# Optimization experiments

Measured on AMD Instinct MI355X. Metric: run time of the kernel, lower is better.

## Reference

```python
import jax, jax.numpy as jnp
import numpy as np

ND, NPROT, E = 50000, 50000, 600000
DIN, DH, DO = 128, 128, 64


def setup_inputs() -> dict:
    key = jax.random.key(0)
    ks = jax.random.split(key, 16)
    s = 0.05
    inp = {
        "x_drug": jax.random.normal(ks[0], (ND, DIN), jnp.float32),
        "x_prot": jax.random.normal(ks[1], (NPROT, DIN), jnp.float32),
        "src_ddi": jax.random.randint(ks[2], (E,), 0, ND, dtype=jnp.int32),
        "dst_ddi": jax.random.randint(ks[3], (E,), 0, ND, dtype=jnp.int32),
        "src_dpi": jax.random.randint(ks[4], (E,), 0, ND, dtype=jnp.int32),
        "dst_dpi": jax.random.randint(ks[5], (E,), 0, NPROT, dtype=jnp.int32),
        "src_ppi": jax.random.randint(ks[6], (E,), 0, NPROT, dtype=jnp.int32),
        "dst_ppi": jax.random.randint(ks[7], (E,), 0, NPROT, dtype=jnp.int32),
        "W1_ddi": jax.random.normal(ks[8], (DIN, DH), jnp.float32) * s,
        "b1_ddi": jnp.zeros((DH,), jnp.float32),
        "W1_dpi": jax.random.normal(ks[9], (DIN, DH), jnp.float32) * s,
        "b1_dpi": jnp.zeros((DH,), jnp.float32),
        "W1_ppi": jax.random.normal(ks[10], (DIN, DH), jnp.float32) * s,
        "b1_ppi": jnp.zeros((DH,), jnp.float32),
        "W2_ddi": jax.random.normal(ks[11], (DH, DO), jnp.float32) * s,
        "b2_ddi": jnp.zeros((DO,), jnp.float32),
        "W2_dpi": jax.random.normal(ks[12], (DH, DO), jnp.float32) * s,
        "b2_dpi": jnp.zeros((DO,), jnp.float32),
        "W2_ppi": jax.random.normal(ks[13], (DH, DO), jnp.float32) * s,
        "b2_ppi": jnp.zeros((DO,), jnp.float32),
    }
    return inp


def _gconv(x_src, src, dst, W, b, n_dst):
    # GraphConv(norm='right'): transform, gather src, sum over in-edges, / in-degree, + bias
    h = x_src @ W                                    # [N_src, dout]
    agg = jax.ops.segment_sum(h[src], dst, num_segments=n_dst)  # [n_dst, dout]
    deg = jax.ops.segment_sum(jnp.ones(src.shape, h.dtype), dst, num_segments=n_dst)
    return agg / jnp.maximum(deg, 1.0)[:, None] + b


def reference(x_drug, x_prot, src_ddi, dst_ddi, src_dpi, dst_dpi, src_ppi, dst_ppi,
              W1_ddi, b1_ddi, W1_dpi, b1_dpi, W1_ppi, b1_ppi,
              W2_ddi, b2_ddi, W2_dpi, b2_dpi, W2_ppi, b2_ppi):
    nd, npr = x_drug.shape[0], x_prot.shape[0]
    # layer 1 (HeteroGraphConv: sum over relations per dst node type)
    h_d = _gconv(x_drug, src_ddi, dst_ddi, W1_ddi, b1_ddi, nd)
    h_p = (_gconv(x_drug, src_dpi, dst_dpi, W1_dpi, b1_dpi, npr)
           + _gconv(x_prot, src_ppi, dst_ppi, W1_ppi, b1_ppi, npr))
    # layer 2
    o_d = _gconv(h_d, src_ddi, dst_ddi, W2_ddi, b2_ddi, nd)
    o_p = (_gconv(h_d, src_dpi, dst_dpi, W2_dpi, b2_dpi, npr)
           + _gconv(h_p, src_ppi, dst_ppi, W2_ppi, b2_ppi, npr))
    # concat drug | protein outputs into one array
    return jnp.concatenate([o_d, o_p], axis=0)
```

## Files before the change

### kernel.cpp

```cpp
#include <hip/hip_runtime.h>

typedef unsigned int uint32;
typedef unsigned short ushort16;
typedef unsigned long long u64;
using short8 = __attribute__((ext_vector_type(8))) short;
using f32x4  = __attribute__((ext_vector_type(4))) float;

__device__ __forceinline__ float bfl(uint32 v) { return __uint_as_float(v << 16); }
__device__ __forceinline__ float bfh(uint32 v) { return __uint_as_float(v & 0xffff0000u); }
__device__ __forceinline__ ushort16 f2bf(float f) {
    uint32 u = __float_as_uint(f);
    u += 0x7fffu + ((u >> 16) & 1u);
    return (ushort16)(u >> 16);
}
__device__ __forceinline__ uint32 pack2(float x, float y) {
    return (uint32)f2bf(x) | ((uint32)f2bf(y) << 16);
}


constexpr int BIN_SH   = 10;
constexpr int CAP_PAIR = 16384;
constexpr int LCAP     = 48;
constexpr int NBIN_MAX = 160;

__global__ void init_ccur_kernel(int* __restrict__ ccur, int nbin) {
    int b = threadIdx.x;
    if (b < nbin) ccur[b] = b * CAP_PAIR;
}

__global__ __launch_bounds__(256) void part_a_kernel(
        const int* __restrict__ s0, const int* __restrict__ d0,
        const int* __restrict__ s1, const int* __restrict__ d1,
        const int* __restrict__ s2, const int* __restrict__ d2,
        int e0, int e01, int e012, int o1, int o2, int nbin,
        int* __restrict__ ccur, u64* __restrict__ cpair) {
    __shared__ u64 buf[NBIN_MAX][LCAP];
    __shared__ int lcnt[NBIN_MAX];
    const int tid = threadIdx.x;
    for (int b = tid; b < nbin; b += 256) lcnt[b] = 0;
    __syncthreads();
    const int step = gridDim.x * 1024;
    for (int base = blockIdx.x * 1024; base < e012; base += step) {
        #pragma unroll
        for (int k = 0; k < 4; ++k) {
            int i = base + tid + k * 256;
            if (i < e012) {
                int g, sv;
                if (i < e0)       { g = d0[i];            sv = s0[i]; }
                else if (i < e01) { g = o1 + d1[i - e0];  sv = s1[i - e0]; }
                else              { g = o2 + d2[i - e01]; sv = s2[i - e01]; }
                int bin = g >> BIN_SH;
                u64 pr = ((u64)(uint32)g << 32) | (uint32)sv;
                int slot = atomicAdd(&lcnt[bin], 1);
                if (slot < LCAP) {
                    buf[bin][slot] = pr;
                } else {
                    int p = atomicAdd(&ccur[bin], 1);
                    cpair[p] = pr;
                    atomicSub(&lcnt[bin], 1);
                }
            }
        }
        __syncthreads();
        if (tid < nbin) {
            int cnt = min(lcnt[tid], LCAP);
            if (cnt >= 32) {
                int n = cnt & ~31;
                int p = atomicAdd(&ccur[tid], n);
                for (int k = 0; k < n; ++k) cpair[p + k] = buf[tid][k];
                for (int k = 0; k < cnt - n; ++k) buf[tid][k] = buf[tid][n + k];
                lcnt[tid] = cnt - n;
            }
        }
        __syncthreads();
    }
    if (tid < nbin) {
        int cnt = min(lcnt[tid], LCAP);
        if (cnt > 0) {
            int p = atomicAdd(&ccur[tid], cnt);
            for (int k = 0; k < cnt; ++k) cpair[p + k] = buf[tid][k];
        }
    }
}

__global__ __launch_bounds__(64) void scan_bins_kernel(const int* __restrict__ ccur, int nbin,
                                                       int* __restrict__ cofs) {
    int lane = threadIdx.x;
    int run = 0;
    for (int base = 0; base < nbin; base += 64) {
        int b = base + lane;
        int c = (b < nbin) ? (ccur[b] - b * CAP_PAIR) : 0;
        int v = c;
        #pragma unroll
        for (int off = 1; off < 64; off <<= 1) {
            int u = __shfl_up(v, off);
            if (lane >= off) v += u;
        }
        if (b < nbin) cofs[b] = run + (v - c);
        run += __shfl(v, 63);
    }
    if (lane == 0) cofs[nbin] = run;
}

__global__ __launch_bounds__(256) void part_b_kernel(const u64* __restrict__ cpair,
                                                     const int* __restrict__ cofs,
                                                     int nbin, int tn, int e012,
                                                     int* __restrict__ rs,
                                                     int* __restrict__ esrc) {
    __shared__ int rs_l[1024];
    __shared__ int cur_l[1024];
    __shared__ int tsum[256];
    const int bin = blockIdx.x;
    const int t = threadIdx.x;
    const int g0 = bin << BIN_SH;
    const int gcnt = min(1024, tn - g0);
    const int pbase = bin * CAP_PAIR;
    const int obase = cofs[bin];
    const int cnt = cofs[bin + 1] - obase;
    #pragma unroll
    for (int k = 0; k < 4; ++k) cur_l[t + k * 256] = 0;
    __syncthreads();
    for (int i = t; i < cnt; i += 256) {
        int g = (int)(cpair[pbase + i] >> 32);
        atomicAdd(&cur_l[g - g0], 1);
    }
    __syncthreads();
    int v[4]; int s = 0;
    #pragma unroll
    for (int k = 0; k < 4; ++k) { v[k] = cur_l[t * 4 + k]; s += v[k]; }
    tsum[t] = s;
    __syncthreads();
    for (int off = 1; off < 256; off <<= 1) {
        int add = (t >= off) ? tsum[t - off] : 0;
        __syncthreads();
        tsum[t] += add;
        __syncthreads();
    }
    int run = (t ? tsum[t - 1] : 0);
    #pragma unroll
    for (int k = 0; k < 4; ++k) { rs_l[t * 4 + k] = run; run += v[k]; }
    __syncthreads();
    #pragma unroll
    for (int k = 0; k < 4; ++k) {
        int j = t + k * 256;
        if (j < gcnt) rs[g0 + j] = obase + rs_l[j];
    }
    if (bin == nbin - 1 && t == 0) rs[tn] = e012;
    #pragma unroll
    for (int k = 0; k < 4; ++k) cur_l[t + k * 256] = 0;
    __syncthreads();
    for (int i = t; i < cnt; i += 256) {
        u64 pr = cpair[pbase + i];
        int g = (int)(pr >> 32);
        int p = atomicAdd(&cur_l[g - g0], 1);
        esrc[obase + rs_l[g - g0] + p] = (int)(uint32)(pr & 0xffffffffu);
    }
}


struct CvtWArgs { const float* W[6]; ushort16* Wt[6]; };

__global__ void cvtW_all_kernel(CvtWArgs a) {
    int i = blockIdx.x * blockDim.x + threadIdx.x;
    if (i < 3 * 16384) {
        int m = i / 16384, idx = i % 16384;
        int n = idx >> 7, k = idx & 127;
        a.Wt[m][n * 128 + k] = f2bf(a.W[m][k * 128 + n]);
    } else {
        i -= 3 * 16384;
        if (i >= 3 * 8192) return;
        int m = 3 + i / 8192, idx = i % 8192;
        int n = idx >> 7, k = idx & 127;
        a.Wt[m][n * 128 + k] = f2bf(a.W[m][k * 64 + n]);
    }
}


struct Gemm3Args {
    const void* A[3];
    const ushort16* Wt[3];
    ushort16* Y[3];
    int N[3];
    int nb0, nb01;
};

template<int M, bool F32A>
__global__ __launch_bounds__(256) void gemm3_kernel(Gemm3Args g) {
    constexpr int NTW = M / 64;
    constexpr int CH  = M / 8;
    __shared__ short8 As[64 * 16];
    int b = blockIdx.x;
    int r = (b < g.nb0) ? 0 : ((b < g.nb01) ? 1 : 2);
    int bloc = b - ((r == 0) ? 0 : ((r == 1) ? g.nb0 : g.nb01));
    const int N = g.N[r];
    const int row0 = bloc * 64;
    const int tid = threadIdx.x;
    const int w = tid >> 6, l = tid & 63;
    const int lr = l & 15, lg = l >> 4;

    #pragma unroll
    for (int it = 0; it < 4; ++it) {
        int idx = it * 256 + tid;
        int row = idx >> 4, c = idx & 15;
        int grow = row0 + row;
        short8 v = {0, 0, 0, 0, 0, 0, 0, 0};
        if (grow < N) {
            if (F32A) {
                const float* gp = (const float*)g.A[r] + (size_t)grow * 128 + c * 8;
                float4 f0 = *(const float4*)gp;
                float4 f1 = *(const float4*)(gp + 4);
                v[0] = (short)f2bf(f0.x); v[1] = (short)f2bf(f0.y);
                v[2] = (short)f2bf(f0.z); v[3] = (short)f2bf(f0.w);
                v[4] = (short)f2bf(f1.x); v[5] = (short)f2bf(f1.y);
                v[6] = (short)f2bf(f1.z); v[7] = (short)f2bf(f1.w);
            } else {
                v = *(const short8*)((const ushort16*)g.A[r] + (size_t)grow * 128 + c * 8);
            }
        }
        As[row * 16 + (c ^ (row & 7))] = v;
    }
    __syncthreads();

    short8 bf[NTW][4];
    #pragma unroll
    for (int t = 0; t < NTW; ++t) {
        int n = w * (NTW * 16) + t * 16 + lr;
        const ushort16* wr = g.Wt[r] + (size_t)n * 128 + lg * 8;
        #pragma unroll
        for (int ks = 0; ks < 4; ++ks) bf[t][ks] = *(const short8*)(wr + ks * 32);
    }

    f32x4 acc[4][NTW];
    #pragma unroll
    for (int rt = 0; rt < 4; ++rt)
        #pragma unroll
        for (int t = 0; t < NTW; ++t) acc[rt][t] = (f32x4){0.f, 0.f, 0.f, 0.f};

    #pragma unroll
    for (int rt = 0; rt < 4; ++rt) {
        int row = rt * 16 + lr;
        short8 a[4];
        #pragma unroll
        for (int ks = 0; ks < 4; ++ks)
            a[ks] = As[row * 16 + ((lg + ks * 4) ^ (lr & 7))];
        #pragma unroll
        for (int t = 0; t < NTW; ++t)
            #pragma unroll
            for (int ks = 0; ks < 4; ++ks)
                acc[rt][t] = __builtin_amdgcn_mfma_f32_16x16x32_bf16(a[ks], bf[t][ks],
                                                                     acc[rt][t], 0, 0, 0);
    }

    __syncthreads();
    ushort16* Ys = (ushort16*)As;
    #pragma unroll
    for (int rt = 0; rt < 4; ++rt) {
        int row = rt * 16 + lg * 4;
        #pragma unroll
        for (int t = 0; t < NTW; ++t) {
            int col = w * (NTW * 16) + t * 16 + lr;
            int chx = (col >> 3);
            #pragma unroll
            for (int j = 0; j < 4; ++j) {
                int rr = row + j;
                Ys[rr * M + ((chx ^ (rr & 7)) << 3) + (col & 7)] = f2bf(acc[rt][t][j]);
            }
        }
    }
    __syncthreads();
    ushort16* Y = g.Y[r];
    #pragma unroll
    for (int it = 0; it < 64 * CH / 256; ++it) {
        int idx = it * 256 + tid;
        int row = idx / CH, c = idx % CH;
        int grow = row0 + row;
        if (grow < N) {
            short8 v = *(const short8*)&Ys[row * M + ((c ^ (row & 7)) << 3)];
            *(short8*)(Y + (size_t)grow * M + c * 8) = v;
        }
    }
}


__global__ __launch_bounds__(256) void agg1_kernel(const uint4* __restrict__ tbA,
                                                   const uint4* __restrict__ tbB,
                                                   const uint4* __restrict__ tbC,
                                                   const int* __restrict__ esrc,
                                                   const int* __restrict__ rs,
                                                   const float* __restrict__ bA,
                                                   const float* __restrict__ bB,
                                                   const float* __restrict__ bC,
                                                   uint4* __restrict__ hd,
                                                   uint4* __restrict__ hp,
                                                   int ND, int NP, int o1, int o2) {
    __shared__ int sidx[4][64];
    const int w = threadIdx.x >> 6;
    const int lane = threadIdx.x & 63;
    const int wid = blockIdx.x * 4 + w;
    const int q = lane >> 4, c = lane & 15;
    if (wid >= ND + NP) return;
    float acc[8];
    auto zero = [&]() {
        for (int k = 0; k < 8; ++k) acc[k] = 0.f;
    };
    auto gather = [&](const uint4* __restrict__ tb, int e0, int e1) {
        for (int base = e0; base < e1; base += 64) {
            int cnt = min(64, e1 - base);
            if (lane < cnt) sidx[w][lane] = esrc[base + lane];
            int j = q;
            for (; j + 4 < cnt; j += 8) {
                uint4 v0 = tb[(size_t)sidx[w][j] * 16 + c];
                uint4 v1 = tb[(size_t)sidx[w][j + 4] * 16 + c];
                acc[0] += bfl(v0.x) + bfl(v1.x);  acc[1] += bfh(v0.x) + bfh(v1.x);
                acc[2] += bfl(v0.y) + bfl(v1.y);  acc[3] += bfh(v0.y) + bfh(v1.y);
                acc[4] += bfl(v0.z) + bfl(v1.z);  acc[5] += bfh(v0.z) + bfh(v1.z);
                acc[6] += bfl(v0.w) + bfl(v1.w);  acc[7] += bfh(v0.w) + bfh(v1.w);
            }
            if (j < cnt) {
                uint4 v0 = tb[(size_t)sidx[w][j] * 16 + c];
                acc[0] += bfl(v0.x);  acc[1] += bfh(v0.x);
                acc[2] += bfl(v0.y);  acc[3] += bfh(v0.y);
                acc[4] += bfl(v0.z);  acc[5] += bfh(v0.z);
                acc[6] += bfl(v0.w);  acc[7] += bfh(v0.w);
            }
        }
        #pragma unroll
        for (int k = 0; k < 8; ++k) {
            acc[k] += __shfl_xor(acc[k], 16);
            acc[k] += __shfl_xor(acc[k], 32);
        }
    };
    if (wid < ND) {
        int e0 = rs[wid], e1 = rs[wid + 1];
        zero();
        gather(tbA, e0, e1);
        if (lane < 16) {
            float inv = 1.f / (float)max(e1 - e0, 1);
            float4 b0 = ((const float4*)bA)[c * 2];
            float4 b1 = ((const float4*)bA)[c * 2 + 1];
            hd[(size_t)wid * 16 + c] = make_uint4(
                pack2(acc[0] * inv + b0.x, acc[1] * inv + b0.y),
                pack2(acc[2] * inv + b0.z, acc[3] * inv + b0.w),
                pack2(acc[4] * inv + b1.x, acc[5] * inv + b1.y),
                pack2(acc[6] * inv + b1.z, acc[7] * inv + b1.w));
        }
    } else {
        int p = wid - ND;
        int g1 = o1 + p, g2 = o2 + p;
        int e0 = rs[g1], e1 = rs[g1 + 1];
        zero();
        gather(tbB, e0, e1);
        float res[8];
        float inv1 = 1.f / (float)max(e1 - e0, 1);
        #pragma unroll
        for (int k = 0; k < 8; ++k) res[k] = acc[k] * inv1;
        int f0 = rs[g2], f1 = rs[g2 + 1];
        zero();
        gather(tbC, f0, f1);
        if (lane < 16) {
            float inv2 = 1.f / (float)max(f1 - f0, 1);
            float4 bb0 = ((const float4*)bB)[c * 2];
            float4 bb1 = ((const float4*)bB)[c * 2 + 1];
            float4 bc0 = ((const float4*)bC)[c * 2];
            float4 bc1 = ((const float4*)bC)[c * 2 + 1];
            float r0 = res[0] + acc[0] * inv2 + bb0.x + bc0.x;
            float r1 = res[1] + acc[1] * inv2 + bb0.y + bc0.y;
            float r2 = res[2] + acc[2] * inv2 + bb0.z + bc0.z;
            float r3 = res[3] + acc[3] * inv2 + bb0.w + bc0.w;
            float r4 = res[4] + acc[4] * inv2 + bb1.x + bc1.x;
            float r5 = res[5] + acc[5] * inv2 + bb1.y + bc1.y;
            float r6 = res[6] + acc[6] * inv2 + bb1.z + bc1.z;
            float r7 = res[7] + acc[7] * inv2 + bb1.w + bc1.w;
            hp[(size_t)p * 16 + c] = make_uint4(pack2(r0, r1), pack2(r2, r3),
                                                pack2(r4, r5), pack2(r6, r7));
        }
    }
}

__global__ __launch_bounds__(256) void agg2_kernel(const uint4* __restrict__ tbA,
                                                   const uint4* __restrict__ tbB,
                                                   const uint4* __restrict__ tbC,
                                                   const int* __restrict__ esrc,
                                                   const int* __restrict__ rs,
                                                   const float* __restrict__ bA,
                                                   const float* __restrict__ bB,
                                                   const float* __restrict__ bC,
                                                   float* __restrict__ out,
                                                   int ND, int NP, int o1, int o2) {
    __shared__ int sidx[4][64];
    const int w = threadIdx.x >> 6;
    const int lane = threadIdx.x & 63;
    const int wid = blockIdx.x * 4 + w;
    const int e8 = lane >> 3, c = lane & 7;
    if (wid >= ND + NP) return;
    float acc[8];
    auto zero = [&]() {
        for (int k = 0; k < 8; ++k) acc[k] = 0.f;
    };
    auto gather = [&](const uint4* __restrict__ tb, int e0, int e1) {
        for (int base = e0; base < e1; base += 64) {
            int cnt = min(64, e1 - base);
            if (lane < cnt) sidx[w][lane] = esrc[base + lane];
            int j = e8;
            for (; j + 8 < cnt; j += 16) {
                uint4 v0 = tb[(size_t)sidx[w][j] * 8 + c];
                uint4 v1 = tb[(size_t)sidx[w][j + 8] * 8 + c];
                acc[0] += bfl(v0.x) + bfl(v1.x);  acc[1] += bfh(v0.x) + bfh(v1.x);
                acc[2] += bfl(v0.y) + bfl(v1.y);  acc[3] += bfh(v0.y) + bfh(v1.y);
                acc[4] += bfl(v0.z) + bfl(v1.z);  acc[5] += bfh(v0.z) + bfh(v1.z);
                acc[6] += bfl(v0.w) + bfl(v1.w);  acc[7] += bfh(v0.w) + bfh(v1.w);
            }
            if (j < cnt) {
                uint4 v0 = tb[(size_t)sidx[w][j] * 8 + c];
                acc[0] += bfl(v0.x);  acc[1] += bfh(v0.x);
                acc[2] += bfl(v0.y);  acc[3] += bfh(v0.y);
                acc[4] += bfl(v0.z);  acc[5] += bfh(v0.z);
                acc[6] += bfl(v0.w);  acc[7] += bfh(v0.w);
            }
        }
        #pragma unroll
        for (int k = 0; k < 8; ++k) {
            acc[k] += __shfl_xor(acc[k], 8);
            acc[k] += __shfl_xor(acc[k], 16);
            acc[k] += __shfl_xor(acc[k], 32);
        }
    };
    if (wid < ND) {
        int e0 = rs[wid], e1 = rs[wid + 1];
        zero();
        gather(tbA, e0, e1);
        if (lane < 8) {
            float inv = 1.f / (float)max(e1 - e0, 1);
            float4 b0 = ((const float4*)bA)[c * 2];
            float4 b1 = ((const float4*)bA)[c * 2 + 1];
            float4 r0, r1;
            r0.x = acc[0] * inv + b0.x; r0.y = acc[1] * inv + b0.y;
            r0.z = acc[2] * inv + b0.z; r0.w = acc[3] * inv + b0.w;
            r1.x = acc[4] * inv + b1.x; r1.y = acc[5] * inv + b1.y;
            r1.z = acc[6] * inv + b1.z; r1.w = acc[7] * inv + b1.w;
            float4* op = (float4*)out + (size_t)wid * 16 + c * 2;
            op[0] = r0; op[1] = r1;
        }
    } else {
        int p = wid - ND;
        int g1 = o1 + p, g2 = o2 + p;
        int e0 = rs[g1], e1 = rs[g1 + 1];
        zero();
        gather(tbB, e0, e1);
        float res[8];
        float inv1 = 1.f / (float)max(e1 - e0, 1);
        #pragma unroll
        for (int k = 0; k < 8; ++k) res[k] = acc[k] * inv1;
        int f0 = rs[g2], f1 = rs[g2 + 1];
        zero();
        gather(tbC, f0, f1);
        if (lane < 8) {
            float inv2 = 1.f / (float)max(f1 - f0, 1);
            float4 bb0 = ((const float4*)bB)[c * 2];
            float4 bb1 = ((const float4*)bB)[c * 2 + 1];
            float4 bc0 = ((const float4*)bC)[c * 2];
            float4 bc1 = ((const float4*)bC)[c * 2 + 1];
            float4 r0, r1;
            r0.x = res[0] + acc[0] * inv2 + bb0.x + bc0.x;
            r0.y = res[1] + acc[1] * inv2 + bb0.y + bc0.y;
            r0.z = res[2] + acc[2] * inv2 + bb0.z + bc0.z;
            r0.w = res[3] + acc[3] * inv2 + bb0.w + bc0.w;
            r1.x = res[4] + acc[4] * inv2 + bb1.x + bc1.x;
            r1.y = res[5] + acc[5] * inv2 + bb1.y + bc1.y;
            r1.z = res[6] + acc[6] * inv2 + bb1.z + bc1.z;
            r1.w = res[7] + acc[7] * inv2 + bb1.w + bc1.w;
            float4* op = (float4*)out + (size_t)(ND + p) * 16 + c * 2;
            op[0] = r0; op[1] = r1;
        }
    }
}


extern "C" void kernel_launch(void* const* d_in, const int* in_sizes, int n_in,
                              void* d_out, int out_size, void* d_ws, size_t ws_size,
                              hipStream_t stream) {
    const float* x_drug = (const float*)d_in[0];
    const float* x_prot = (const float*)d_in[1];
    const int* src[3] = { (const int*)d_in[2], (const int*)d_in[4], (const int*)d_in[6] };
    const int* dst[3] = { (const int*)d_in[3], (const int*)d_in[5], (const int*)d_in[7] };
    const float* W1[3] = { (const float*)d_in[8],  (const float*)d_in[10], (const float*)d_in[12] };
    const float* b1[3] = { (const float*)d_in[9],  (const float*)d_in[11], (const float*)d_in[13] };
    const float* W2[3] = { (const float*)d_in[14], (const float*)d_in[16], (const float*)d_in[18] };
    const float* b2[3] = { (const float*)d_in[15], (const float*)d_in[17], (const float*)d_in[19] };

    const int ND = in_sizes[0] / 128;
    const int NP = in_sizes[1] / 128;
    const int EC[3] = { in_sizes[2], in_sizes[4], in_sizes[6] };
    float* out = (float*)d_out;

    const int o1 = ND, o2 = ND + NP;
    const int TN = ND + 2 * NP;
    const int NBIN = (TN + (1 << BIN_SH) - 1) >> BIN_SH;
    const int e0c = EC[0], e01 = EC[0] + EC[1], e012 = EC[0] + EC[1] + EC[2];

    char* w = (char*)d_ws;
    ushort16* hd16 = (ushort16*)w; w += (size_t)ND * 128 * 2;
    ushort16* hp16 = (ushort16*)w; w += (size_t)NP * 128 * 2;
    ushort16* tbA  = (ushort16*)w; w += (size_t)ND * 128 * 2;
    ushort16* tbB  = (ushort16*)w; w += (size_t)ND * 128 * 2;
    ushort16* tbC  = (ushort16*)w; w += (size_t)NP * 128 * 2;
    ushort16* Wt[6];
    for (int r = 0; r < 3; ++r) { Wt[r] = (ushort16*)w; w += 128 * 128 * 2; }
    for (int r = 0; r < 3; ++r) { Wt[3 + r] = (ushort16*)w; w += 64 * 128 * 2; }
    int* ip = (int*)w;
    int* rs_all   = ip; ip += TN + 1;
    int* esrc_all = ip; ip += e012;
    int* ccur     = ip; ip += NBIN_MAX;
    int* cofs     = ip; ip += NBIN_MAX + 1;
    u64* cpair = (u64*)hd16;

    {
        CvtWArgs a;
        for (int r = 0; r < 3; ++r) { a.W[r] = W1[r]; a.W[3 + r] = W2[r]; }
        for (int r = 0; r < 6; ++r) a.Wt[r] = Wt[r];
        cvtW_all_kernel<<<(3 * 16384 + 3 * 8192 + 255) / 256, 256, 0, stream>>>(a);
    }

    init_ccur_kernel<<<1, 256, 0, stream>>>(ccur, NBIN);
    part_a_kernel<<<512, 256, 0, stream>>>(src[0], dst[0], src[1], dst[1], src[2], dst[2],
                                           e0c, e01, e012, o1, o2, NBIN, ccur, cpair);
    scan_bins_kernel<<<1, 64, 0, stream>>>(ccur, NBIN, cofs);
    part_b_kernel<<<NBIN, 256, 0, stream>>>(cpair, cofs, NBIN, TN, e012, rs_all, esrc_all);

    auto gb64 = [](int n) { return (n + 63) / 64; };
    auto ab = [](int n) { return (n + 3) / 4; };

    {
        Gemm3Args g;
        g.A[0] = x_drug; g.A[1] = x_drug; g.A[2] = x_prot;
        g.Wt[0] = Wt[0]; g.Wt[1] = Wt[1]; g.Wt[2] = Wt[2];
        g.Y[0] = tbA; g.Y[1] = tbB; g.Y[2] = tbC;
        g.N[0] = ND; g.N[1] = ND; g.N[2] = NP;
        g.nb0 = gb64(ND); g.nb01 = gb64(ND) * 2;
        int nblk = gb64(ND) * 2 + gb64(NP);
        gemm3_kernel<128, true><<<nblk, 256, 0, stream>>>(g);
    }
    agg1_kernel<<<ab(ND + NP), 256, 0, stream>>>((const uint4*)tbA, (const uint4*)tbB,
                                                 (const uint4*)tbC, esrc_all, rs_all,
                                                 b1[0], b1[1], b1[2],
                                                 (uint4*)hd16, (uint4*)hp16, ND, NP, o1, o2);

    {
        Gemm3Args g;
        g.A[0] = hd16; g.A[1] = hd16; g.A[2] = hp16;
        g.Wt[0] = Wt[3]; g.Wt[1] = Wt[4]; g.Wt[2] = Wt[5];
        g.Y[0] = tbA; g.Y[1] = tbB; g.Y[2] = tbC;
        g.N[0] = ND; g.N[1] = ND; g.N[2] = NP;
        g.nb0 = gb64(ND); g.nb01 = gb64(ND) * 2;
        int nblk = gb64(ND) * 2 + gb64(NP);
        gemm3_kernel<64, false><<<nblk, 256, 0, stream>>>(g);
    }
    agg2_kernel<<<ab(ND + NP), 256, 0, stream>>>((const uint4*)tbA, (const uint4*)tbB,
                                                 (const uint4*)tbC, esrc_all, rs_all,
                                                 b2[0], b2[1], b2[2],
                                                 out, ND, NP, o1, o2);
}
```

Baseline: 244.5 us.

## Replace buffered binning with histogram-scan-scatter and fuse scatter into layer-1 GEMM launch

Replaces the shared-memory buffered bin partition with a deterministic per-block histogram, a flat prefix scan, and an exact-offset scatter. The weight conversion is folded into the histogram kernel. The scatter blocks share one launch with the layer-1 GEMM blocks so the two independent workloads can overlap. This removes the init kernel and the fixed-capacity padded pair layout, at the cost of reading dst twice and running a single-block 1024-thread scan over about 40K counters.

```diff
diff --git a/kernel.cpp b/kernel.cpp
--- a/kernel.cpp
+++ b/kernel.cpp
@@ -19,160 +19,77 @@
 
 
 constexpr int BIN_SH   = 10;
-constexpr int CAP_PAIR = 16384;
-constexpr int LCAP     = 48;
 constexpr int NBIN_MAX = 160;
-
-__global__ void init_ccur_kernel(int* __restrict__ ccur, int nbin) {
-    int b = threadIdx.x;
-    if (b < nbin) ccur[b] = b * CAP_PAIR;
-}
-
-__global__ __launch_bounds__(256) void part_a_kernel(
-        const int* __restrict__ s0, const int* __restrict__ d0,
-        const int* __restrict__ s1, const int* __restrict__ d1,
-        const int* __restrict__ s2, const int* __restrict__ d2,
+constexpr int PG       = 256;
+
+struct CvtWArgs { const float* W[6]; ushort16* Wt[6]; };
+
+__global__ __launch_bounds__(256) void hist_cvtw_kernel(
+        const int* __restrict__ d0, const int* __restrict__ d1, const int* __restrict__ d2,
         int e0, int e01, int e012, int o1, int o2, int nbin,
-        int* __restrict__ ccur, u64* __restrict__ cpair) {
-    __shared__ u64 buf[NBIN_MAX][LCAP];
-    __shared__ int lcnt[NBIN_MAX];
+        int* __restrict__ cntmat, CvtWArgs a) {
+    __shared__ int hist[NBIN_MAX];
     const int tid = threadIdx.x;
-    for (int b = tid; b < nbin; b += 256) lcnt[b] = 0;
-    __syncthreads();
-    const int step = gridDim.x * 1024;
-    for (int base = blockIdx.x * 1024; base < e012; base += step) {
+    const int blk = blockIdx.x;
+    for (int b = tid; b < nbin; b += 256) hist[b] = 0;
+    __syncthreads();
+    const int step = PG * 1024;
+    for (int base = blk * 1024; base < e012; base += step) {
         #pragma unroll
         for (int k = 0; k < 4; ++k) {
             int i = base + tid + k * 256;
             if (i < e012) {
-                int g, sv;
-                if (i < e0)       { g = d0[i];            sv = s0[i]; }
-                else if (i < e01) { g = o1 + d1[i - e0];  sv = s1[i - e0]; }
-                else              { g = o2 + d2[i - e01]; sv = s2[i - e01]; }
-                int bin = g >> BIN_SH;
-                u64 pr = ((u64)(uint32)g << 32) | (uint32)sv;
-                int slot = atomicAdd(&lcnt[bin], 1);
-                if (slot < LCAP) {
-                    buf[bin][slot] = pr;
-                } else {
-                    int p = atomicAdd(&ccur[bin], 1);
-                    cpair[p] = pr;
-                    atomicSub(&lcnt[bin], 1);
-                }
-            }
-        }
-        __syncthreads();
-        if (tid < nbin) {
-            int cnt = min(lcnt[tid], LCAP);
-            if (cnt >= 32) {
-                int n = cnt & ~31;
-                int p = atomicAdd(&ccur[tid], n);
-                for (int k = 0; k < n; ++k) cpair[p + k] = buf[tid][k];
-                for (int k = 0; k < cnt - n; ++k) buf[tid][k] = buf[tid][n + k];
-                lcnt[tid] = cnt - n;
-            }
-        }
-        __syncthreads();
-    }
-    if (tid < nbin) {
-        int cnt = min(lcnt[tid], LCAP);
-        if (cnt > 0) {
-            int p = atomicAdd(&ccur[tid], cnt);
-            for (int k = 0; k < cnt; ++k) cpair[p + k] = buf[tid][k];
-        }
-    }
-}
-
-__global__ __launch_bounds__(64) void scan_bins_kernel(const int* __restrict__ ccur, int nbin,
-                                                       int* __restrict__ cofs) {
-    int lane = threadIdx.x;
-    int run = 0;
-    for (int base = 0; base < nbin; base += 64) {
-        int b = base + lane;
-        int c = (b < nbin) ? (ccur[b] - b * CAP_PAIR) : 0;
-        int v = c;
-        #pragma unroll
-        for (int off = 1; off < 64; off <<= 1) {
-            int u = __shfl_up(v, off);
-            if (lane >= off) v += u;
-        }
-        if (b < nbin) cofs[b] = run + (v - c);
-        run += __shfl(v, 63);
-    }
-    if (lane == 0) cofs[nbin] = run;
-}
-
-__global__ __launch_bounds__(256) void part_b_kernel(const u64* __restrict__ cpair,
-                                                     const int* __restrict__ cofs,
-                                                     int nbin, int tn, int e012,
-                                                     int* __restrict__ rs,
-                                                     int* __restrict__ esrc) {
-    __shared__ int rs_l[1024];
-    __shared__ int cur_l[1024];
-    __shared__ int tsum[256];
-    const int bin = blockIdx.x;
+                int g;
+                if (i < e0)       g = d0[i];
+                else if (i < e01) g = o1 + d1[i - e0];
+                else              g = o2 + d2[i - e01];
+                atomicAdd(&hist[g >> BIN_SH], 1);
+            }
+        }
+    }
+    __syncthreads();
+    for (int b = tid; b < nbin; b += 256) cntmat[b * PG + blk] = hist[b];
+    const int gid = blk * 256 + tid;
+    for (int i = gid; i < 3 * 16384 + 3 * 8192; i += PG * 256) {
+        if (i < 3 * 16384) {
+            int m = i / 16384, idx = i % 16384;
+            int n = idx >> 7, k = idx & 127;
+            a.Wt[m][n * 128 + k] = f2bf(a.W[m][k * 128 + n]);
+        } else {
+            int j = i - 3 * 16384;
+            int m = 3 + j / 8192, idx = j % 8192;
+            int n = idx >> 7, k = idx & 127;
+            a.Wt[m][n * 128 + k] = f2bf(a.W[m][k * 64 + n]);
+        }
+    }
+}
+
+__global__ __launch_bounds__(1024) void scanflat_kernel(const int* __restrict__ cntmat,
+                                                        int n, int nbin,
+                                                        int* __restrict__ soff,
+                                                        int* __restrict__ cofs) {
+    __shared__ int tsum[1024];
     const int t = threadIdx.x;
-    const int g0 = bin << BIN_SH;
-    const int gcnt = min(1024, tn - g0);
-    const int pbase = bin * CAP_PAIR;
-    const int obase = cofs[bin];
-    const int cnt = cofs[bin + 1] - obase;
-    #pragma unroll
-    for (int k = 0; k < 4; ++k) cur_l[t + k * 256] = 0;
-    __syncthreads();
-    for (int i = t; i < cnt; i += 256) {
-        int g = (int)(cpair[pbase + i] >> 32);
-        atomicAdd(&cur_l[g - g0], 1);
-    }
-    __syncthreads();
-    int v[4]; int s = 0;
-    #pragma unroll
-    for (int k = 0; k < 4; ++k) { v[k] = cur_l[t * 4 + k]; s += v[k]; }
+    const int vpt = (n + 1023) >> 10;
+    const int lo = min(t * vpt, n);
+    const int hi = min(lo + vpt, n);
+    int s = 0;
+    for (int i = lo; i < hi; ++i) s += cntmat[i];
     tsum[t] = s;
     __syncthreads();
-    for (int off = 1; off < 256; off <<= 1) {
+    for (int off = 1; off < 1024; off <<= 1) {
         int add = (t >= off) ? tsum[t - off] : 0;
         __syncthreads();
         tsum[t] += add;
         __syncthreads();
     }
     int run = (t ? tsum[t - 1] : 0);
-    #pragma unroll
-    for (int k = 0; k < 4; ++k) { rs_l[t * 4 + k] = run; run += v[k]; }
-    __syncthreads();
-    #pragma unroll
-    for (int k = 0; k < 4; ++k) {
-        int j = t + k * 256;
-        if (j < gcnt) rs[g0 + j] = obase + rs_l[j];
-    }
-    if (bin == nbin - 1 && t == 0) rs[tn] = e012;
-    #pragma unroll
-    for (int k = 0; k < 4; ++k) cur_l[t + k * 256] = 0;
-    __syncthreads();
-    for (int i = t; i < cnt; i += 256) {
-        u64 pr = cpair[pbase + i];
-        int g = (int)(pr >> 32);
-        int p = atomicAdd(&cur_l[g - g0], 1);
-        esrc[obase + rs_l[g - g0] + p] = (int)(uint32)(pr & 0xffffffffu);
-    }
-}
-
-
-struct CvtWArgs { const float* W[6]; ushort16* Wt[6]; };
-
-__global__ void cvtW_all_kernel(CvtWArgs a) {
-    int i = blockIdx.x * blockDim.x + threadIdx.x;
-    if (i < 3 * 16384) {
-        int m = i / 16384, idx = i % 16384;
-        int n = idx >> 7, k = idx & 127;
-        a.Wt[m][n * 128 + k] = f2bf(a.W[m][k * 128 + n]);
-    } else {
-        i -= 3 * 16384;
-        if (i >= 3 * 8192) return;
-        int m = 3 + i / 8192, idx = i % 8192;
-        int n = idx >> 7, k = idx & 127;
-        a.Wt[m][n * 128 + k] = f2bf(a.W[m][k * 64 + n]);
-    }
+    for (int i = lo; i < hi; ++i) {
+        soff[i] = run;
+        if ((i & (PG - 1)) == 0) cofs[i / PG] = run;
+        run += cntmat[i];
+    }
+    if (t == 1023) cofs[nbin] = tsum[1023];
 }
 
 
@@ -185,11 +102,10 @@
 };
 
 template<int M, bool F32A>
-__global__ __launch_bounds__(256) void gemm3_kernel(Gemm3Args g) {
+__device__ __forceinline__ void gemm3_body(const Gemm3Args& g, int b, char* smem) {
     constexpr int NTW = M / 64;
     constexpr int CH  = M / 8;
-    __shared__ short8 As[64 * 16];
-    int b = blockIdx.x;
+    short8* As = (short8*)smem;
     int r = (b < g.nb0) ? 0 : ((b < g.nb01) ? 1 : 2);
     int bloc = b - ((r == 0) ? 0 : ((r == 1) ? g.nb0 : g.nb01));
     const int N = g.N[r];
@@ -252,7 +168,7 @@
     }
 
     __syncthreads();
-    ushort16* Ys = (ushort16*)As;
+    ushort16* Ys = (ushort16*)smem;
     #pragma unroll
     for (int rt = 0; rt < 4; ++rt) {
         int row = rt * 16 + lg * 4;
@@ -278,6 +194,101 @@
             short8 v = *(const short8*)&Ys[row * M + ((c ^ (row & 7)) << 3)];
             *(short8*)(Y + (size_t)grow * M + c * 8) = v;
         }
+    }
+}
+
+template<int M, bool F32A>
+__global__ __launch_bounds__(256) void a3gemm_kernel(
+        const int* __restrict__ s0, const int* __restrict__ d0,
+        const int* __restrict__ s1, const int* __restrict__ d1,
+        const int* __restrict__ s2, const int* __restrict__ d2,
+        int e0, int e01, int e012, int o1, int o2, int nbin,
+        const int* __restrict__ soff, u64* __restrict__ cpair,
+        Gemm3Args g) {
+    __shared__ char smem[16384];
+    const int tid = threadIdx.x;
+    if (blockIdx.x < PG) {
+        int* lcnt = (int*)smem;
+        const int blk = blockIdx.x;
+        for (int b = tid; b < nbin; b += 256) lcnt[b] = soff[b * PG + blk];
+        __syncthreads();
+        const int step = PG * 1024;
+        for (int base = blk * 1024; base < e012; base += step) {
+            #pragma unroll
+            for (int k = 0; k < 4; ++k) {
+                int i = base + tid + k * 256;
+                if (i < e012) {
+                    int gg, sv;
+                    if (i < e0)       { gg = d0[i];            sv = s0[i]; }
+                    else if (i < e01) { gg = o1 + d1[i - e0];  sv = s1[i - e0]; }
+                    else              { gg = o2 + d2[i - e01]; sv = s2[i - e01]; }
+                    int p = atomicAdd(&lcnt[gg >> BIN_SH], 1);
+                    cpair[p] = ((u64)(uint32)gg << 32) | (uint32)sv;
+                }
+            }
+        }
+    } else {
+        gemm3_body<M, F32A>(g, blockIdx.x - PG, smem);
+    }
+}
+
+template<int M, bool F32A>
+__global__ __launch_bounds__(256) void gemm3_kernel(Gemm3Args g) {
+    __shared__ char smem[16384];
+    gemm3_body<M, F32A>(g, blockIdx.x, smem);
+}
+
+__global__ __launch_bounds__(256) void part_b_kernel(const u64* __restrict__ cpair,
+                                                     const int* __restrict__ cofs,
+                                                     int nbin, int tn, int e012,
+                                                     int* __restrict__ rs,
+                                                     int* __restrict__ esrc) {
+    __shared__ int rs_l[1024];
+    __shared__ int cur_l[1024];
+    __shared__ int tsum[256];
+    const int bin = blockIdx.x;
+    const int t = threadIdx.x;
+    const int g0 = bin << BIN_SH;
+    const int gcnt = min(1024, tn - g0);
+    const int pbase = cofs[bin];
+    const int cnt = cofs[bin + 1] - pbase;
+    #pragma unroll
+    for (int k = 0; k < 4; ++k) cur_l[t + k * 256] = 0;
+    __syncthreads();
+    for (int i = t; i < cnt; i += 256) {
+        int g = (int)(cpair[pbase + i] >> 32);
+        atomicAdd(&cur_l[g - g0], 1);
+    }
+    __syncthreads();
+    int v[4]; int s = 0;
+    #pragma unroll
+    for (int k = 0; k < 4; ++k) { v[k] = cur_l[t * 4 + k]; s += v[k]; }
+    tsum[t] = s;
+    __syncthreads();
+    for (int off = 1; off < 256; off <<= 1) {
+        int add = (t >= off) ? tsum[t - off] : 0;
+        __syncthreads();
+        tsum[t] += add;
+        __syncthreads();
+    }
+    int run = (t ? tsum[t - 1] : 0);
+    #pragma unroll
+    for (int k = 0; k < 4; ++k) { rs_l[t * 4 + k] = run; run += v[k]; }
+    __syncthreads();
+    #pragma unroll
+    for (int k = 0; k < 4; ++k) {
+        int j = t + k * 256;
+        if (j < gcnt) rs[g0 + j] = pbase + rs_l[j];
+    }
+    if (bin == nbin - 1 && t == 0) rs[tn] = e012;
+    #pragma unroll
+    for (int k = 0; k < 4; ++k) cur_l[t + k * 256] = 0;
+    __syncthreads();
+    for (int i = t; i < cnt; i += 256) {
+        u64 pr = cpair[pbase + i];
+        int g = (int)(pr >> 32);
+        int p = atomicAdd(&cur_l[g - g0], 1);
+        esrc[pbase + rs_l[g - g0] + p] = (int)(uint32)(pr & 0xffffffffu);
     }
 }
 
@@ -510,51 +521,49 @@
     int* ip = (int*)w;
     int* rs_all   = ip; ip += TN + 1;
     int* esrc_all = ip; ip += e012;
-    int* ccur     = ip; ip += NBIN_MAX;
+    int* cntmat   = ip; ip += NBIN_MAX * PG;
+    int* soff     = ip; ip += NBIN_MAX * PG;
     int* cofs     = ip; ip += NBIN_MAX + 1;
     u64* cpair = (u64*)hd16;
 
-    {
-        CvtWArgs a;
-        for (int r = 0; r < 3; ++r) { a.W[r] = W1[r]; a.W[3 + r] = W2[r]; }
-        for (int r = 0; r < 6; ++r) a.Wt[r] = Wt[r];
-        cvtW_all_kernel<<<(3 * 16384 + 3 * 8192 + 255) / 256, 256, 0, stream>>>(a);
-    }
-
-    init_ccur_kernel<<<1, 256, 0, stream>>>(ccur, NBIN);
-    part_a_kernel<<<512, 256, 0, stream>>>(src[0], dst[0], src[1], dst[1], src[2], dst[2],
-                                           e0c, e01, e012, o1, o2, NBIN, ccur, cpair);
-    scan_bins_kernel<<<1, 64, 0, stream>>>(ccur, NBIN, cofs);
-    part_b_kernel<<<NBIN, 256, 0, stream>>>(cpair, cofs, NBIN, TN, e012, rs_all, esrc_all);
-
     auto gb64 = [](int n) { return (n + 63) / 64; };
     auto ab = [](int n) { return (n + 3) / 4; };
 
-    {
-        Gemm3Args g;
-        g.A[0] = x_drug; g.A[1] = x_drug; g.A[2] = x_prot;
-        g.Wt[0] = Wt[0]; g.Wt[1] = Wt[1]; g.Wt[2] = Wt[2];
-        g.Y[0] = tbA; g.Y[1] = tbB; g.Y[2] = tbC;
-        g.N[0] = ND; g.N[1] = ND; g.N[2] = NP;
-        g.nb0 = gb64(ND); g.nb01 = gb64(ND) * 2;
-        int nblk = gb64(ND) * 2 + gb64(NP);
-        gemm3_kernel<128, true><<<nblk, 256, 0, stream>>>(g);
-    }
+    CvtWArgs cw;
+    for (int r = 0; r < 3; ++r) { cw.W[r] = W1[r]; cw.W[3 + r] = W2[r]; }
+    for (int r = 0; r < 6; ++r) cw.Wt[r] = Wt[r];
+    hist_cvtw_kernel<<<PG, 256, 0, stream>>>(dst[0], dst[1], dst[2],
+                                             e0c, e01, e012, o1, o2, NBIN, cntmat, cw);
+
+    scanflat_kernel<<<1, 1024, 0, stream>>>(cntmat, NBIN * PG, NBIN, soff, cofs);
+
+    Gemm3Args g1;
+    g1.A[0] = x_drug; g1.A[1] = x_drug; g1.A[2] = x_prot;
+    g1.Wt[0] = Wt[0]; g1.Wt[1] = Wt[1]; g1.Wt[2] = Wt[2];
+    g1.Y[0] = tbA; g1.Y[1] = tbB; g1.Y[2] = tbC;
+    g1.N[0] = ND; g1.N[1] = ND; g1.N[2] = NP;
+    g1.nb0 = gb64(ND); g1.nb01 = gb64(ND) * 2;
+    int nblk1 = gb64(ND) * 2 + gb64(NP);
+    a3gemm_kernel<128, true><<<PG + nblk1, 256, 0, stream>>>(
+        src[0], dst[0], src[1], dst[1], src[2], dst[2],
+        e0c, e01, e012, o1, o2, NBIN, soff, cpair, g1);
+
+    part_b_kernel<<<NBIN, 256, 0, stream>>>(cpair, cofs, NBIN, TN, e012, rs_all, esrc_all);
+
     agg1_kernel<<<ab(ND + NP), 256, 0, stream>>>((const uint4*)tbA, (const uint4*)tbB,
                                                  (const uint4*)tbC, esrc_all, rs_all,
                                                  b1[0], b1[1], b1[2],
                                                  (uint4*)hd16, (uint4*)hp16, ND, NP, o1, o2);
 
-    {
-        Gemm3Args g;
-        g.A[0] = hd16; g.A[1] = hd16; g.A[2] = hp16;
-        g.Wt[0] = Wt[3]; g.Wt[1] = Wt[4]; g.Wt[2] = Wt[5];
-        g.Y[0] = tbA; g.Y[1] = tbB; g.Y[2] = tbC;
-        g.N[0] = ND; g.N[1] = ND; g.N[2] = NP;
-        g.nb0 = gb64(ND); g.nb01 = gb64(ND) * 2;
-        int nblk = gb64(ND) * 2 + gb64(NP);
-        gemm3_kernel<64, false><<<nblk, 256, 0, stream>>>(g);
-    }
+    Gemm3Args g2;
+    g2.A[0] = hd16; g2.A[1] = hd16; g2.A[2] = hp16;
+    g2.Wt[0] = Wt[3]; g2.Wt[1] = Wt[4]; g2.Wt[2] = Wt[5];
+    g2.Y[0] = tbA; g2.Y[1] = tbB; g2.Y[2] = tbC;
+    g2.N[0] = ND; g2.N[1] = ND; g2.N[2] = NP;
+    g2.nb0 = gb64(ND); g2.nb01 = gb64(ND) * 2;
+    int nblk2 = gb64(ND) * 2 + gb64(NP);
+    gemm3_kernel<64, false><<<nblk2, 256, 0, stream>>>(g2);
+
     agg2_kernel<<<ab(ND + NP), 256, 0, stream>>>((const uint4*)tbA, (const uint4*)tbB,
                                                  (const uint4*)tbC, esrc_all, rs_all,
                                                  b2[0], b2[1], b2[2],
```

Result: slower. 268.9 us (+10.0%).
